# Kernel optimization log

Hardware: AMD Instinct MI355X
Metric: run time of the kernel (lower is better)

The kernel has to match this reference:

```python
import jax, jax.numpy as jnp
import numpy as np

N_T = 2_000_000      # terrain nodes
E_SEQ = 2_000_000    # sequence edges
E_AS = 2_000_000     # assignment edges
N_TOR = 1_000_000    # torus nodes
E_TR = 8_000_000     # transport edges
TD, OD, PD, N_OPS = 4, 3, 1, 4  # terrain dim, torus dim, polarity dim, num operators


def setup_inputs() -> dict:
    key = jax.random.key(0)
    ks = jax.random.split(key, 12)
    inp = {
        "x_terrain": jax.random.normal(ks[0], (N_T, TD), jnp.float32),
        "polarity": jax.random.normal(ks[1], (E_AS, PD), jnp.float32),
        "x_torus": jax.random.normal(ks[2], (N_TOR, OD), jnp.float32),
        "seq_ei": jax.random.randint(ks[3], (2, E_SEQ), 0, N_T),
        "assign_src": jax.random.randint(ks[4], (E_AS,), 0, N_T),
        "assign_dst": jax.random.randint(ks[5], (E_AS,), 0, N_OPS),
        "tr_ei": jax.random.randint(ks[6], (2, E_TR), 0, N_TOR),
        # learned params (nn.Linear convention: y = x @ W.T + b)
        "W_seq": jax.random.normal(ks[7], (TD, TD), jnp.float32) * 0.5,      # SequenceConv.lin, no bias
        "op_W": jax.random.normal(ks[8], (N_OPS, TD, TD + PD), jnp.float32) * 0.4,
        "op_b": jax.random.normal(ks[9], (N_OPS, TD), jnp.float32) * 0.1,
        "gate_W": jax.random.normal(ks[10], (2 * OD, 1), jnp.float32) * 0.4,  # TransportConv.gate
        "gate_b": jax.random.normal(ks[11], (1,), jnp.float32) * 0.1,
    }
    return inp


def _engine_fwd(x_terrain, polarity, x_torus, W_seq, op_W, op_b, gate_W, gate_b,
                seq_ei, assign_src, assign_dst, tr_ei):
    # 1) SequenceConv: add-aggregated linear message along terrain cycle, residual add
    msg = x_terrain[seq_ei[0]] @ W_seq.T                       # [E_seq, TD]
    agg = jnp.zeros_like(x_terrain).at[seq_ei[1]].add(msg)     # scatter-add to dst
    x_t = x_terrain + agg

    # 2) per-node operator transform: first assignment edge per source node
    E = assign_src.shape[0]
    pos = jnp.arange(E, dtype=jnp.int32)
    first = jax.ops.segment_min(pos, assign_src, num_segments=x_t.shape[0])  # fill = int32 max
    has = first < E                                            # nodes with >=1 assignment
    fe = jnp.clip(first, 0, E - 1)
    op_idx = jnp.clip(assign_dst[fe], 0, op_W.shape[0] - 1)    # [N_T]
    pol = polarity[fe]                                         # [N_T, 1]
    inp = jnp.concatenate([x_t, pol], axis=-1)                 # [N_T, TD+1]
    out = jnp.einsum('nij,nj->ni', op_W[op_idx], inp) + op_b[op_idx]
    x_t = jnp.where(has[:, None], out, x_t)

    # 3) TransportConv: sigmoid-gated mean aggregation over torus edges, residual add
    src, dst = tr_ei[0], tr_ei[1]
    xi, xj = x_torus[dst], x_torus[src]
    gate = jax.nn.sigmoid(jnp.concatenate([xi, xj], axis=-1) @ gate_W + gate_b)  # [E_tr,1]
    m = gate * xj
    s = jax.ops.segment_sum(m, dst, num_segments=x_torus.shape[0])
    cnt = jax.ops.segment_sum(jnp.ones((m.shape[0],), m.dtype), dst,
                              num_segments=x_torus.shape[0])
    x_tor = x_torus + s / jnp.maximum(cnt, 1.0)[:, None]
    return x_t, x_tor


def reference(x_terrain, polarity, x_torus, seq_ei, assign_src, assign_dst, tr_ei,
              W_seq, op_W, op_b, gate_W, gate_b):
    return _engine_fwd(x_terrain, polarity, x_torus, W_seq, op_W, op_b, gate_W, gate_b,
                       seq_ei, assign_src, assign_dst, tr_ei)
```

## Files before the change

kernel.cpp:

```cpp
#include <hip/hip_runtime.h>
#include <hip/hip_fp16.h>
#include <math.h>

#define N_T   2000000
#define E_SEQ 2000000
#define E_AS  2000000
#define N_TOR 1000000
#define E_TR  8000000
#define NREP  8

typedef unsigned long long u64;

__device__ __forceinline__ long long center_field(u64 t, int bits) {
    long long h = 1LL << (bits - 1);
    return (long long)((t & ((1ULL << bits) - 1)) ^ (u64)h) - h;
}

__device__ __forceinline__ unsigned xcc_id() {
    return __builtin_amdgcn_s_getreg((3 << 11) | 20) & 7u;
}

__global__ __launch_bounds__(256) void initA_kernel(ulonglong2* __restrict__ a,
                                                    ulonglong2* __restrict__ b) {
    long long i = (long long)blockIdx.x * blockDim.x + threadIdx.x;
    if (i < 2500000LL) a[i] = make_ulonglong2(0, 0);
    else if (i < 4000000LL) b[i - 2500000LL] = make_ulonglong2(0, 0);
}

__global__ __launch_bounds__(256) void prep_kernel(
        const float* __restrict__ x_torus,
        const float* __restrict__ gate_W, const float* __restrict__ gate_b,
        u64* __restrict__ src_pk, float* __restrict__ yi_arr) {
    int n = blockIdx.x * blockDim.x + threadIdx.x;
    if (n >= N_TOR) return;
    const float* x = x_torus + (size_t)n * 3;
    float x0 = x[0], x1 = x[1], x2 = x[2];
    float yi = fmaf(x0, gate_W[0], fmaf(x1, gate_W[1], x2 * gate_W[2]));
    float yj = fmaf(x0, gate_W[3], fmaf(x1, gate_W[4], fmaf(x2, gate_W[5], gate_b[0])));
    unsigned short u0, u1, u2, u3;
    __half h;
    h = __float2half(x0); __builtin_memcpy(&u0, &h, 2);
    h = __float2half(x1); __builtin_memcpy(&u1, &h, 2);
    h = __float2half(x2); __builtin_memcpy(&u2, &h, 2);
    h = __float2half(yj); __builtin_memcpy(&u3, &h, 2);
    src_pk[n] = (u64)u0 | ((u64)u1 << 16) | ((u64)u2 << 32) | ((u64)u3 << 48);
    yi_arr[n] = yi;
}

__global__ __launch_bounds__(256) void tr_kernel(
        const int* __restrict__ tr_src, const int* __restrict__ tr_dst,
        const u64* __restrict__ src_pk, const float* __restrict__ yi_arr,
        u64* rep_ws, u64* rep_out) {
    int e = blockIdx.x * blockDim.x + threadIdx.x;
    if (e >= E_TR) return;
    int si = __builtin_nontemporal_load(tr_src + e);
    int di = __builtin_nontemporal_load(tr_dst + e);
    u64 s = __builtin_nontemporal_load(src_pk + si);
    unsigned short u0 = (unsigned short)s, u1 = (unsigned short)(s >> 16),
                   u2 = (unsigned short)(s >> 32), u3 = (unsigned short)(s >> 48);
    __half h0, h1, h2, h3;
    __builtin_memcpy(&h0, &u0, 2); __builtin_memcpy(&h1, &u1, 2);
    __builtin_memcpy(&h2, &u2, 2); __builtin_memcpy(&h3, &u3, 2);
    float x0 = __half2float(h0), x1 = __half2float(h1), x2 = __half2float(h2);
    float z = yi_arr[di] + __half2float(h3);
    float g = 1.0f / (1.0f + __expf(-z));
    long long f0 = __float2int_rn(g * x0 * 128.0f);
    long long f1 = __float2int_rn(g * x1 * 128.0f);
    long long f2 = __float2int_rn(g * x2 * 128.0f);
    long long pk = f0 + (f1 << 17) + (f2 << 34) + (1LL << 51);
    unsigned r = xcc_id();
    u64* rep = (r < 5) ? rep_ws + (size_t)r * N_TOR
                       : rep_out + (size_t)(r - 5) * N_TOR;
    __hip_atomic_fetch_add(&rep[di], (u64)pk, __ATOMIC_RELAXED,
                           __HIP_MEMORY_SCOPE_WORKGROUP);
}

__global__ __launch_bounds__(256) void reduce_kernel(
        const u64* rep_ws, const u64* rep_out, u64* tor_sum) {
    int n = blockIdx.x * blockDim.x + threadIdx.x;
    if (n >= N_TOR) return;
    u64 t = 0;
    #pragma unroll
    for (int r = 0; r < 5; ++r) t += rep_ws[(size_t)r * N_TOR + n];
    #pragma unroll
    for (int r = 0; r < 3; ++r) t += rep_out[(size_t)r * N_TOR + n];
    tor_sum[n] = t;
}

__global__ __launch_bounds__(256) void initB_kernel(ulonglong2* __restrict__ ws) {
    long long i = (long long)blockIdx.x * blockDim.x + threadIdx.x;
    if (i >= 2000000LL) return;
    u64 v = (i * 2 < (long long)N_T) ? 0ULL : ~0ULL;
    ws[i] = make_ulonglong2(v, v);
}

__global__ __launch_bounds__(256) void sa_kernel(
        const float4* __restrict__ x_terrain,
        const int* __restrict__ seq_src, const int* __restrict__ seq_dst,
        const float* __restrict__ W_seq, u64* __restrict__ agg_pk,
        const int* __restrict__ assign_src, const int* __restrict__ assign_dst,
        const float* __restrict__ polarity, u64* __restrict__ first_pk) {
    int i = blockIdx.x * blockDim.x + threadIdx.x;
    if (i < E_SEQ) {
        int e = i;
        int s = __builtin_nontemporal_load(seq_src + e);
        int d = __builtin_nontemporal_load(seq_dst + e);
        float4 x = x_terrain[s];
        float m0 = fmaf(x.x, W_seq[0],  fmaf(x.y, W_seq[1],  fmaf(x.z, W_seq[2],  x.w * W_seq[3])));
        float m1 = fmaf(x.x, W_seq[4],  fmaf(x.y, W_seq[5],  fmaf(x.z, W_seq[6],  x.w * W_seq[7])));
        float m2 = fmaf(x.x, W_seq[8],  fmaf(x.y, W_seq[9],  fmaf(x.z, W_seq[10], x.w * W_seq[11])));
        float m3 = fmaf(x.x, W_seq[12], fmaf(x.y, W_seq[13], fmaf(x.z, W_seq[14], x.w * W_seq[15])));
        long long f0 = __float2int_rn(m0 * 256.0f);
        long long f1 = __float2int_rn(m1 * 256.0f);
        long long f2 = __float2int_rn(m2 * 256.0f);
        long long f3 = __float2int_rn(m3 * 256.0f);
        long long pk = f0 + (f1 << 16) + (f2 << 32) + (f3 << 48);
        atomicAdd(&agg_pk[d], (u64)pk);
    } else if (i < E_SEQ + E_AS) {
        int e = i - E_SEQ;
        int op = __builtin_nontemporal_load(assign_dst + e) & 3;
        __half h = __float2half(__builtin_nontemporal_load(polarity + e));
        unsigned short hb;
        __builtin_memcpy(&hb, &h, 2);
        u64 key = ((u64)e << 18) | ((u64)op << 16) | (u64)hb;
        atomicMin(&first_pk[__builtin_nontemporal_load(assign_src + e)], key);
    }
}

__global__ __launch_bounds__(256) void node_kernel(
        const float4* __restrict__ x_terrain,
        const u64* __restrict__ agg_pk,
        const u64* __restrict__ first_pk,
        const float* __restrict__ op_W, const float* __restrict__ op_b,
        float4* __restrict__ out_xt,
        const float* __restrict__ x_torus,
        const u64* __restrict__ tor_sum,
        float* __restrict__ out_tor) {
    int i = blockIdx.x * blockDim.x + threadIdx.x;
    if (i < N_T) {
        int n = i;
        float4 x = x_terrain[n];
        u64 t = agg_pk[n];
        long long m0 = center_field(t, 16); t = (t - (u64)m0) >> 16;
        long long m1 = center_field(t, 16); t = (t - (u64)m1) >> 16;
        long long m2 = center_field(t, 16); t = (t - (u64)m2) >> 16;
        long long m3 = center_field(t, 16);
        const float inv = 1.0f / 256.0f;
        x.x += (float)m0 * inv; x.y += (float)m1 * inv;
        x.z += (float)m2 * inv; x.w += (float)m3 * inv;
        u64 fp = first_pk[n];
        if ((fp >> 18) < (u64)E_AS) {
            int op = (int)((fp >> 16) & 3);
            unsigned short hb = (unsigned short)(fp & 0xFFFF);
            __half h;
            __builtin_memcpy(&h, &hb, 2);
            float pol = __half2float(h);
            const float* W = op_W + op * 20;
            const float* b = op_b + op * 4;
            float4 o;
            o.x = fmaf(x.x, W[0],  fmaf(x.y, W[1],  fmaf(x.z, W[2],  fmaf(x.w, W[3],  fmaf(pol, W[4],  b[0])))));
            o.y = fmaf(x.x, W[5],  fmaf(x.y, W[6],  fmaf(x.z, W[7],  fmaf(x.w, W[8],  fmaf(pol, W[9],  b[1])))));
            o.z = fmaf(x.x, W[10], fmaf(x.y, W[11], fmaf(x.z, W[12], fmaf(x.w, W[13], fmaf(pol, W[14], b[2])))));
            o.w = fmaf(x.x, W[15], fmaf(x.y, W[16], fmaf(x.z, W[17], fmaf(x.w, W[18], fmaf(pol, W[19], b[3])))));
            x = o;
        }
        out_xt[n] = x;
    } else if (i < N_T + N_TOR) {
        int n = i - N_T;
        u64 t = tor_sum[n];
        long long m0 = center_field(t, 17); t = (t - (u64)m0) >> 17;
        long long m1 = center_field(t, 17); t = (t - (u64)m1) >> 17;
        long long m2 = center_field(t, 17); t = (t - (u64)m2) >> 17;
        float cnt = (float)(t & 0x1FFF);
        float inv = (1.0f / 128.0f) / fmaxf(cnt, 1.0f);
        size_t b = (size_t)n * 3;
        out_tor[b + 0] = x_torus[b + 0] + (float)m0 * inv;
        out_tor[b + 1] = x_torus[b + 1] + (float)m1 * inv;
        out_tor[b + 2] = x_torus[b + 2] + (float)m2 * inv;
    }
}

extern "C" void kernel_launch(void* const* d_in, const int* in_sizes, int n_in,
                              void* d_out, int out_size, void* d_ws, size_t ws_size,
                              hipStream_t stream) {
    const float* x_terrain  = (const float*)d_in[0];
    const float* polarity   = (const float*)d_in[1];
    const float* x_torus    = (const float*)d_in[2];
    const int*   seq_ei     = (const int*)  d_in[3];
    const int*   assign_src = (const int*)  d_in[4];
    const int*   assign_dst = (const int*)  d_in[5];
    const int*   tr_ei      = (const int*)  d_in[6];
    const float* W_seq      = (const float*)d_in[7];
    const float* op_W       = (const float*)d_in[8];
    const float* op_b       = (const float*)d_in[9];
    const float* gate_W     = (const float*)d_in[10];
    const float* gate_b     = (const float*)d_in[11];

    float* out_xt  = (float*)d_out;
    float* out_tor = (float*)d_out + (size_t)N_T * 4;

    u64* wsu      = (u64*)d_ws;
    u64* rep_ws   = wsu;
    u64* agg_pk   = wsu;
    u64* first_pk = wsu + N_T;
    u64* tor_sum  = wsu + 2 * (size_t)N_T;
    u64* rep_out  = (u64*)d_out;
    u64* src_pk   = (u64*)d_out + 3 * (size_t)N_TOR;
    float* yi_arr = (float*)((u64*)d_out + 4 * (size_t)N_TOR);

    const int B = 256;
    initA_kernel<<<(4000000 + B - 1) / B, B, 0, stream>>>(
        (ulonglong2*)rep_ws, (ulonglong2*)rep_out);
    prep_kernel<<<(N_TOR + B - 1) / B, B, 0, stream>>>(
        x_torus, gate_W, gate_b, src_pk, yi_arr);
    tr_kernel<<<(E_TR + B - 1) / B, B, 0, stream>>>(
        tr_ei, tr_ei + E_TR, src_pk, yi_arr, rep_ws, rep_out);
    reduce_kernel<<<(N_TOR + B - 1) / B, B, 0, stream>>>(
        rep_ws, rep_out, tor_sum);
    initB_kernel<<<(2000000 + B - 1) / B, B, 0, stream>>>((ulonglong2*)wsu);
    sa_kernel<<<((E_SEQ + E_AS) + B - 1) / B, B, 0, stream>>>(
        (const float4*)x_terrain, seq_ei, seq_ei + E_SEQ, W_seq, agg_pk,
        assign_src, assign_dst, polarity, first_pk);
    const long long total_n = (long long)N_T + N_TOR;
    node_kernel<<<(int)((total_n + B - 1) / B), B, 0, stream>>>(
        (const float4*)x_terrain, agg_pk, first_pk, op_W, op_b, (float4*)out_xt,
        x_torus, tor_sum, out_tor);
}
```

Baseline: 737.6 us.

## Replace replicated global atomics for transport conv with bucketed counting-sort scatter

The transport aggregation drops per-XCC replicated global 64-bit atomics plus a reduce pass. In their place, edges are binned by destination range (histogram, scan, scatter into per-bucket record arrays). Each bucket is then reduced in LDS with shared-memory atomics and written straight to the output, so the torus finalisation leaves node_kernel. This trades random global atomics for an extra pass over the edge stream, 12-bit clamped fixed-point fields, and a single-block scan whose serial prefix sum could become a bottleneck.

Result: slower. 799.7 us (+8.4%).

```diff
diff --git a/kernel.cpp b/kernel.cpp
--- a/kernel.cpp
+++ b/kernel.cpp
@@ -7,84 +7,161 @@
 #define E_AS  2000000
 #define N_TOR 1000000
 #define E_TR  8000000
-#define NREP  8
+
+#define BKT_SHIFT 11
+#define BKT_RANGE 2048
+#define NBKT 489
+#define HIST_BLOCKS 512
+#define CHUNK 4096
+#define NCHUNK ((E_TR + CHUNK - 1) / CHUNK)
+#define NSPILL_A 4850000u
 
 typedef unsigned long long u64;
+typedef unsigned int u32;
 
 __device__ __forceinline__ long long center_field(u64 t, int bits) {
     long long h = 1LL << (bits - 1);
     return (long long)((t & ((1ULL << bits) - 1)) ^ (u64)h) - h;
 }
-
-__device__ __forceinline__ unsigned xcc_id() {
-    return __builtin_amdgcn_s_getreg((3 << 11) | 20) & 7u;
-}
-
-__global__ __launch_bounds__(256) void initA_kernel(ulonglong2* __restrict__ a,
-                                                    ulonglong2* __restrict__ b) {
-    long long i = (long long)blockIdx.x * blockDim.x + threadIdx.x;
-    if (i < 2500000LL) a[i] = make_ulonglong2(0, 0);
-    else if (i < 4000000LL) b[i - 2500000LL] = make_ulonglong2(0, 0);
-}
-
-__global__ __launch_bounds__(256) void prep_kernel(
+__device__ __forceinline__ int sext12(int v) { return ((v & 0xFFF) ^ 0x800) - 0x800; }
+
+__global__ __launch_bounds__(256) void hist_prep_kernel(
+        const int* __restrict__ tr_dst, u32* __restrict__ bhist,
         const float* __restrict__ x_torus,
         const float* __restrict__ gate_W, const float* __restrict__ gate_b,
         u64* __restrict__ src_pk, float* __restrict__ yi_arr) {
-    int n = blockIdx.x * blockDim.x + threadIdx.x;
-    if (n >= N_TOR) return;
-    const float* x = x_torus + (size_t)n * 3;
-    float x0 = x[0], x1 = x[1], x2 = x[2];
-    float yi = fmaf(x0, gate_W[0], fmaf(x1, gate_W[1], x2 * gate_W[2]));
-    float yj = fmaf(x0, gate_W[3], fmaf(x1, gate_W[4], fmaf(x2, gate_W[5], gate_b[0])));
-    unsigned short u0, u1, u2, u3;
-    __half h;
-    h = __float2half(x0); __builtin_memcpy(&u0, &h, 2);
-    h = __float2half(x1); __builtin_memcpy(&u1, &h, 2);
-    h = __float2half(x2); __builtin_memcpy(&u2, &h, 2);
-    h = __float2half(yj); __builtin_memcpy(&u3, &h, 2);
-    src_pk[n] = (u64)u0 | ((u64)u1 << 16) | ((u64)u2 << 32) | ((u64)u3 << 48);
-    yi_arr[n] = yi;
-}
-
-__global__ __launch_bounds__(256) void tr_kernel(
+    if (blockIdx.x < HIST_BLOCKS) {
+        __shared__ u32 h[NBKT];
+        for (int i = threadIdx.x; i < NBKT; i += 256) h[i] = 0;
+        __syncthreads();
+        for (long long e = (long long)blockIdx.x * 256 + threadIdx.x;
+             e < E_TR; e += (long long)HIST_BLOCKS * 256) {
+            int di = __builtin_nontemporal_load(tr_dst + e);
+            atomicAdd(&h[di >> BKT_SHIFT], 1u);
+        }
+        __syncthreads();
+        for (int i = threadIdx.x; i < NBKT; i += 256)
+            bhist[(size_t)blockIdx.x * NBKT + i] = h[i];
+    } else {
+        int n = (blockIdx.x - HIST_BLOCKS) * 256 + threadIdx.x;
+        if (n >= N_TOR) return;
+        const float* x = x_torus + (size_t)n * 3;
+        float x0 = x[0], x1 = x[1], x2 = x[2];
+        float yi = fmaf(x0, gate_W[0], fmaf(x1, gate_W[1], x2 * gate_W[2]));
+        float yj = fmaf(x0, gate_W[3], fmaf(x1, gate_W[4], fmaf(x2, gate_W[5], gate_b[0])));
+        unsigned short u0, u1, u2, u3;
+        __half h;
+        h = __float2half(x0); __builtin_memcpy(&u0, &h, 2);
+        h = __float2half(x1); __builtin_memcpy(&u1, &h, 2);
+        h = __float2half(x2); __builtin_memcpy(&u2, &h, 2);
+        h = __float2half(yj); __builtin_memcpy(&u3, &h, 2);
+        src_pk[n] = (u64)u0 | ((u64)u1 << 16) | ((u64)u2 << 32) | ((u64)u3 << 48);
+        yi_arr[n] = yi;
+    }
+}
+
+__global__ __launch_bounds__(256) void scan_kernel(
+        const u32* __restrict__ bhist, u32* __restrict__ base,
+        u32* __restrict__ cursors) {
+    __shared__ u32 tot[NBKT];
+    for (int b = threadIdx.x; b < NBKT; b += 256) {
+        u32 s = 0;
+        for (int k = 0; k < HIST_BLOCKS; ++k) s += bhist[(size_t)k * NBKT + b];
+        tot[b] = s;
+    }
+    __syncthreads();
+    if (threadIdx.x == 0) {
+        u32 acc = 0;
+        for (int b = 0; b < NBKT; ++b) { base[b] = acc; acc += tot[b]; }
+        base[NBKT] = acc;
+    }
+    __syncthreads();
+    for (int b = threadIdx.x; b < NBKT; b += 256) cursors[b * 8] = base[b];
+}
+
+__global__ __launch_bounds__(256) void scatter_kernel(
         const int* __restrict__ tr_src, const int* __restrict__ tr_dst,
         const u64* __restrict__ src_pk, const float* __restrict__ yi_arr,
-        u64* rep_ws, u64* rep_out) {
-    int e = blockIdx.x * blockDim.x + threadIdx.x;
-    if (e >= E_TR) return;
-    int si = __builtin_nontemporal_load(tr_src + e);
-    int di = __builtin_nontemporal_load(tr_dst + e);
-    u64 s = __builtin_nontemporal_load(src_pk + si);
-    unsigned short u0 = (unsigned short)s, u1 = (unsigned short)(s >> 16),
-                   u2 = (unsigned short)(s >> 32), u3 = (unsigned short)(s >> 48);
-    __half h0, h1, h2, h3;
-    __builtin_memcpy(&h0, &u0, 2); __builtin_memcpy(&h1, &u1, 2);
-    __builtin_memcpy(&h2, &u2, 2); __builtin_memcpy(&h3, &u3, 2);
-    float x0 = __half2float(h0), x1 = __half2float(h1), x2 = __half2float(h2);
-    float z = yi_arr[di] + __half2float(h3);
-    float g = 1.0f / (1.0f + __expf(-z));
-    long long f0 = __float2int_rn(g * x0 * 128.0f);
-    long long f1 = __float2int_rn(g * x1 * 128.0f);
-    long long f2 = __float2int_rn(g * x2 * 128.0f);
-    long long pk = f0 + (f1 << 17) + (f2 << 34) + (1LL << 51);
-    unsigned r = xcc_id();
-    u64* rep = (r < 5) ? rep_ws + (size_t)r * N_TOR
-                       : rep_out + (size_t)(r - 5) * N_TOR;
-    __hip_atomic_fetch_add(&rep[di], (u64)pk, __ATOMIC_RELAXED,
-                           __HIP_MEMORY_SCOPE_WORKGROUP);
-}
-
-__global__ __launch_bounds__(256) void reduce_kernel(
-        const u64* rep_ws, const u64* rep_out, u64* tor_sum) {
-    int n = blockIdx.x * blockDim.x + threadIdx.x;
-    if (n >= N_TOR) return;
-    u64 t = 0;
-    #pragma unroll
-    for (int r = 0; r < 5; ++r) t += rep_ws[(size_t)r * N_TOR + n];
-    #pragma unroll
-    for (int r = 0; r < 3; ++r) t += rep_out[(size_t)r * N_TOR + n];
-    tor_sum[n] = t;
+        u32* __restrict__ cursors,
+        u64* __restrict__ spillA, u64* __restrict__ spillB) {
+    __shared__ u32 h[NBKT];
+    __shared__ u32 sbase[NBKT];
+    long long e0 = (long long)blockIdx.x * CHUNK;
+    int nE = (int)(((long long)E_TR - e0) < CHUNK ? ((long long)E_TR - e0) : CHUNK);
+    for (int i = threadIdx.x; i < NBKT; i += 256) h[i] = 0;
+    __syncthreads();
+    for (int i = threadIdx.x; i < nE; i += 256) {
+        int di = tr_dst[e0 + i];
+        atomicAdd(&h[di >> BKT_SHIFT], 1u);
+    }
+    __syncthreads();
+    for (int b = threadIdx.x; b < NBKT; b += 256) {
+        u32 c = h[b];
+        sbase[b] = c ? atomicAdd(&cursors[b * 8], c) : 0u;
+        h[b] = 0;
+    }
+    __syncthreads();
+    for (int i = threadIdx.x; i < nE; i += 256) {
+        long long e = e0 + i;
+        int si = tr_src[e];
+        int di = tr_dst[e];
+        int bk = di >> BKT_SHIFT;
+        u64 s = src_pk[si];
+        unsigned short u0 = (unsigned short)s, u1 = (unsigned short)(s >> 16),
+                       u2 = (unsigned short)(s >> 32), u3 = (unsigned short)(s >> 48);
+        __half h0, h1, h2, h3;
+        __builtin_memcpy(&h0, &u0, 2); __builtin_memcpy(&h1, &u1, 2);
+        __builtin_memcpy(&h2, &u2, 2); __builtin_memcpy(&h3, &u3, 2);
+        float x0 = __half2float(h0), x1 = __half2float(h1), x2 = __half2float(h2);
+        float z = yi_arr[di] + __half2float(h3);
+        float g = 1.0f / (1.0f + __expf(-z));
+        int f0 = __float2int_rn(g * x0 * 128.0f);
+        int f1 = __float2int_rn(g * x1 * 128.0f);
+        int f2 = __float2int_rn(g * x2 * 128.0f);
+        f0 = f0 > 2047 ? 2047 : (f0 < -2047 ? -2047 : f0);
+        f1 = f1 > 2047 ? 2047 : (f1 < -2047 ? -2047 : f1);
+        f2 = f2 > 2047 ? 2047 : (f2 < -2047 ? -2047 : f2);
+        u32 rank = atomicAdd(&h[bk], 1u);
+        u32 slot = sbase[bk] + rank;
+        u64 rec = (u64)(f0 & 0xFFF) | ((u64)(f1 & 0xFFF) << 12)
+                | ((u64)(f2 & 0xFFF) << 24) | ((u64)(di & (BKT_RANGE - 1)) << 36);
+        if (slot < NSPILL_A) spillA[slot] = rec;
+        else                 spillB[slot - NSPILL_A] = rec;
+    }
+}
+
+__global__ __launch_bounds__(256) void bucket_kernel(
+        const u32* __restrict__ base,
+        const u64* __restrict__ spillA, const u64* __restrict__ spillB,
+        const float* __restrict__ x_torus, float* __restrict__ out_tor) {
+    __shared__ int s0[BKT_RANGE], s1[BKT_RANGE], s2[BKT_RANGE], sc[BKT_RANGE];
+    for (int i = threadIdx.x; i < BKT_RANGE; i += 256) {
+        s0[i] = 0; s1[i] = 0; s2[i] = 0; sc[i] = 0;
+    }
+    __syncthreads();
+    int b = blockIdx.x;
+    u32 lo = base[b], hi = base[b + 1];
+    for (u32 s = lo + threadIdx.x; s < hi; s += 256) {
+        u64 r = (s < NSPILL_A) ? spillA[s] : spillB[s - NSPILL_A];
+        int f0 = sext12((int)(r & 0xFFF));
+        int f1 = sext12((int)((r >> 12) & 0xFFF));
+        int f2 = sext12((int)((r >> 24) & 0xFFF));
+        int l  = (int)((r >> 36) & (BKT_RANGE - 1));
+        atomicAdd(&s0[l], f0); atomicAdd(&s1[l], f1);
+        atomicAdd(&s2[l], f2); atomicAdd(&sc[l], 1);
+    }
+    __syncthreads();
+    int n0 = b << BKT_SHIFT;
+    for (int i = threadIdx.x; i < BKT_RANGE; i += 256) {
+        int n = n0 + i;
+        if (n < N_TOR) {
+            float inv = (1.0f / 128.0f) / fmaxf((float)sc[i], 1.0f);
+            size_t p = (size_t)n * 3;
+            out_tor[p + 0] = x_torus[p + 0] + (float)s0[i] * inv;
+            out_tor[p + 1] = x_torus[p + 1] + (float)s1[i] * inv;
+            out_tor[p + 2] = x_torus[p + 2] + (float)s2[i] * inv;
+        }
+    }
 }
 
 __global__ __launch_bounds__(256) void initB_kernel(ulonglong2* __restrict__ ws) {
@@ -132,52 +209,35 @@
         const u64* __restrict__ agg_pk,
         const u64* __restrict__ first_pk,
         const float* __restrict__ op_W, const float* __restrict__ op_b,
-        float4* __restrict__ out_xt,
-        const float* __restrict__ x_torus,
-        const u64* __restrict__ tor_sum,
-        float* __restrict__ out_tor) {
-    int i = blockIdx.x * blockDim.x + threadIdx.x;
-    if (i < N_T) {
-        int n = i;
-        float4 x = x_terrain[n];
-        u64 t = agg_pk[n];
-        long long m0 = center_field(t, 16); t = (t - (u64)m0) >> 16;
-        long long m1 = center_field(t, 16); t = (t - (u64)m1) >> 16;
-        long long m2 = center_field(t, 16); t = (t - (u64)m2) >> 16;
-        long long m3 = center_field(t, 16);
-        const float inv = 1.0f / 256.0f;
-        x.x += (float)m0 * inv; x.y += (float)m1 * inv;
-        x.z += (float)m2 * inv; x.w += (float)m3 * inv;
-        u64 fp = first_pk[n];
-        if ((fp >> 18) < (u64)E_AS) {
-            int op = (int)((fp >> 16) & 3);
-            unsigned short hb = (unsigned short)(fp & 0xFFFF);
-            __half h;
-            __builtin_memcpy(&h, &hb, 2);
-            float pol = __half2float(h);
-            const float* W = op_W + op * 20;
-            const float* b = op_b + op * 4;
-            float4 o;
-            o.x = fmaf(x.x, W[0],  fmaf(x.y, W[1],  fmaf(x.z, W[2],  fmaf(x.w, W[3],  fmaf(pol, W[4],  b[0])))));
-            o.y = fmaf(x.x, W[5],  fmaf(x.y, W[6],  fmaf(x.z, W[7],  fmaf(x.w, W[8],  fmaf(pol, W[9],  b[1])))));
-            o.z = fmaf(x.x, W[10], fmaf(x.y, W[11], fmaf(x.z, W[12], fmaf(x.w, W[13], fmaf(pol, W[14], b[2])))));
-            o.w = fmaf(x.x, W[15], fmaf(x.y, W[16], fmaf(x.z, W[17], fmaf(x.w, W[18], fmaf(pol, W[19], b[3])))));
-            x = o;
-        }
-        out_xt[n] = x;
-    } else if (i < N_T + N_TOR) {
-        int n = i - N_T;
-        u64 t = tor_sum[n];
-        long long m0 = center_field(t, 17); t = (t - (u64)m0) >> 17;
-        long long m1 = center_field(t, 17); t = (t - (u64)m1) >> 17;
-        long long m2 = center_field(t, 17); t = (t - (u64)m2) >> 17;
-        float cnt = (float)(t & 0x1FFF);
-        float inv = (1.0f / 128.0f) / fmaxf(cnt, 1.0f);
-        size_t b = (size_t)n * 3;
-        out_tor[b + 0] = x_torus[b + 0] + (float)m0 * inv;
-        out_tor[b + 1] = x_torus[b + 1] + (float)m1 * inv;
-        out_tor[b + 2] = x_torus[b + 2] + (float)m2 * inv;
-    }
+        float4* __restrict__ out_xt) {
+    int n = blockIdx.x * blockDim.x + threadIdx.x;
+    if (n >= N_T) return;
+    float4 x = x_terrain[n];
+    u64 t = agg_pk[n];
+    long long m0 = center_field(t, 16); t = (t - (u64)m0) >> 16;
+    long long m1 = center_field(t, 16); t = (t - (u64)m1) >> 16;
+    long long m2 = center_field(t, 16); t = (t - (u64)m2) >> 16;
+    long long m3 = center_field(t, 16);
+    const float inv = 1.0f / 256.0f;
+    x.x += (float)m0 * inv; x.y += (float)m1 * inv;
+    x.z += (float)m2 * inv; x.w += (float)m3 * inv;
+    u64 fp = first_pk[n];
+    if ((fp >> 18) < (u64)E_AS) {
+        int op = (int)((fp >> 16) & 3);
+        unsigned short hb = (unsigned short)(fp & 0xFFFF);
+        __half h;
+        __builtin_memcpy(&h, &hb, 2);
+        float pol = __half2float(h);
+        const float* W = op_W + op * 20;
+        const float* b = op_b + op * 4;
+        float4 o;
+        o.x = fmaf(x.x, W[0],  fmaf(x.y, W[1],  fmaf(x.z, W[2],  fmaf(x.w, W[3],  fmaf(pol, W[4],  b[0])))));
+        o.y = fmaf(x.x, W[5],  fmaf(x.y, W[6],  fmaf(x.z, W[7],  fmaf(x.w, W[8],  fmaf(pol, W[9],  b[1])))));
+        o.z = fmaf(x.x, W[10], fmaf(x.y, W[11], fmaf(x.z, W[12], fmaf(x.w, W[13], fmaf(pol, W[14], b[2])))));
+        o.w = fmaf(x.x, W[15], fmaf(x.y, W[16], fmaf(x.z, W[17], fmaf(x.w, W[18], fmaf(pol, W[19], b[3])))));
+        x = o;
+    }
+    out_xt[n] = x;
 }
 
 extern "C" void kernel_launch(void* const* d_in, const int* in_sizes, int n_in,
@@ -199,30 +259,29 @@
     float* out_xt  = (float*)d_out;
     float* out_tor = (float*)d_out + (size_t)N_T * 4;
 
-    u64* wsu      = (u64*)d_ws;
-    u64* rep_ws   = wsu;
-    u64* agg_pk   = wsu;
-    u64* first_pk = wsu + N_T;
-    u64* tor_sum  = wsu + 2 * (size_t)N_T;
-    u64* rep_out  = (u64*)d_out;
-    u64* src_pk   = (u64*)d_out + 3 * (size_t)N_TOR;
-    float* yi_arr = (float*)((u64*)d_out + 4 * (size_t)N_TOR);
+    u64* spillA   = (u64*)d_ws;
+    char* tail    = (char*)d_ws + (size_t)NSPILL_A * 8;
+    u32* bhist    = (u32*)tail;
+    u32* base     = (u32*)(tail + (size_t)HIST_BLOCKS * NBKT * 4);
+    u32* cursors  = (u32*)(tail + (size_t)HIST_BLOCKS * NBKT * 4 + 2048);
+    u64* spillB   = (u64*)d_out;
+    u64* src_pk   = (u64*)((char*)d_out + 32000000);
+    float* yi_arr = (float*)((char*)d_out + 40000000);
+    u64* agg_pk   = (u64*)d_ws;
+    u64* first_pk = agg_pk + N_T;
 
     const int B = 256;
-    initA_kernel<<<(4000000 + B - 1) / B, B, 0, stream>>>(
-        (ulonglong2*)rep_ws, (ulonglong2*)rep_out);
-    prep_kernel<<<(N_TOR + B - 1) / B, B, 0, stream>>>(
-        x_torus, gate_W, gate_b, src_pk, yi_arr);
-    tr_kernel<<<(E_TR + B - 1) / B, B, 0, stream>>>(
-        tr_ei, tr_ei + E_TR, src_pk, yi_arr, rep_ws, rep_out);
-    reduce_kernel<<<(N_TOR + B - 1) / B, B, 0, stream>>>(
-        rep_ws, rep_out, tor_sum);
-    initB_kernel<<<(2000000 + B - 1) / B, B, 0, stream>>>((ulonglong2*)wsu);
+    const int prep_blocks = (N_TOR + B - 1) / B;
+    hist_prep_kernel<<<HIST_BLOCKS + prep_blocks, B, 0, stream>>>(
+        tr_ei + E_TR, bhist, x_torus, gate_W, gate_b, src_pk, yi_arr);
+    scan_kernel<<<1, B, 0, stream>>>(bhist, base, cursors);
+    scatter_kernel<<<NCHUNK, B, 0, stream>>>(
+        tr_ei, tr_ei + E_TR, src_pk, yi_arr, cursors, spillA, spillB);
+    bucket_kernel<<<NBKT, B, 0, stream>>>(base, spillA, spillB, x_torus, out_tor);
+    initB_kernel<<<(2000000 + B - 1) / B, B, 0, stream>>>((ulonglong2*)d_ws);
     sa_kernel<<<((E_SEQ + E_AS) + B - 1) / B, B, 0, stream>>>(
         (const float4*)x_terrain, seq_ei, seq_ei + E_SEQ, W_seq, agg_pk,
         assign_src, assign_dst, polarity, first_pk);
-    const long long total_n = (long long)N_T + N_TOR;
-    node_kernel<<<(int)((total_n + B - 1) / B), B, 0, stream>>>(
-        (const float4*)x_terrain, agg_pk, first_pk, op_W, op_b, (float4*)out_xt,
-        x_torus, tor_sum, out_tor);
-}
+    node_kernel<<<(N_T + B - 1) / B, B, 0, stream>>>(
+        (const float4*)x_terrain, agg_pk, first_pk, op_W, op_b, (float4*)out_xt);
+}
```

## Bucket transport edges by destination range and consume per-XCC partitions

Applied to the files above, without the earlier changes.

Replaces the per-XCC replicated atomic accumulators for the torus transport scatter with a two-phase scheme. A build kernel computes gated messages, packs them into 12-bit fixed-point records tagged with the destination, and bins them into eight destination buckets via block-local staging. A consume kernel then has each XCC atomically accumulate only the bucket for its node range, so atomics stay local to one XCC's cache. The change also drops the replica reduce and init kernels and moves the torus finalization into the sa kernel. In exchange it writes and rereads an extra 64 MB record stream, reduces message precision through 12-bit clamping, and depends on xcc_id being 0-7 and on an overflow buffer.

Result: slower. 1.173 ms (+59.0%).

```diff
diff --git a/kernel.cpp b/kernel.cpp
--- a/kernel.cpp
+++ b/kernel.cpp
@@ -7,32 +7,42 @@
 #define E_AS  2000000
 #define N_TOR 1000000
 #define E_TR  8000000
-#define NREP  8
+
+#define NB 8
+#define BKT_NODES 125000
+#define C_BKT 983040u
+#define OVF_CAP 262144u
+#define CHUNK 2048
+#define NCHUNK ((E_TR + CHUNK - 1) / CHUNK)
+
+#define C_CUR    0
+#define C_OVF    8
+#define C_RCLAIM 16
+#define C_OCLAIM 24
 
 typedef unsigned long long u64;
+typedef unsigned int u32;
 
 __device__ __forceinline__ long long center_field(u64 t, int bits) {
     long long h = 1LL << (bits - 1);
     return (long long)((t & ((1ULL << bits) - 1)) ^ (u64)h) - h;
 }
-
+__device__ __forceinline__ long long sext12(int v) {
+    return (long long)(((v & 0xFFF) ^ 0x800) - 0x800);
+}
 __device__ __forceinline__ unsigned xcc_id() {
     return __builtin_amdgcn_s_getreg((3 << 11) | 20) & 7u;
-}
-
-__global__ __launch_bounds__(256) void initA_kernel(ulonglong2* __restrict__ a,
-                                                    ulonglong2* __restrict__ b) {
-    long long i = (long long)blockIdx.x * blockDim.x + threadIdx.x;
-    if (i < 2500000LL) a[i] = make_ulonglong2(0, 0);
-    else if (i < 4000000LL) b[i - 2500000LL] = make_ulonglong2(0, 0);
 }
 
 __global__ __launch_bounds__(256) void prep_kernel(
         const float* __restrict__ x_torus,
         const float* __restrict__ gate_W, const float* __restrict__ gate_b,
-        u64* __restrict__ src_pk, float* __restrict__ yi_arr) {
+        u64* __restrict__ src_pk, __half* __restrict__ yi_h,
+        u64* __restrict__ tor_acc, u32* __restrict__ ctrl) {
     int n = blockIdx.x * blockDim.x + threadIdx.x;
+    if (n < 64) ctrl[n] = 0;
     if (n >= N_TOR) return;
+    tor_acc[n] = 0ULL;
     const float* x = x_torus + (size_t)n * 3;
     float x0 = x[0], x1 = x[1], x2 = x[2];
     float yi = fmaf(x0, gate_W[0], fmaf(x1, gate_W[1], x2 * gate_W[2]));
@@ -44,47 +54,141 @@
     h = __float2half(x2); __builtin_memcpy(&u2, &h, 2);
     h = __float2half(yj); __builtin_memcpy(&u3, &h, 2);
     src_pk[n] = (u64)u0 | ((u64)u1 << 16) | ((u64)u2 << 32) | ((u64)u3 << 48);
-    yi_arr[n] = yi;
-}
-
-__global__ __launch_bounds__(256) void tr_kernel(
+    yi_h[n] = __float2half(yi);
+}
+
+__global__ __launch_bounds__(256) void build_kernel(
         const int* __restrict__ tr_src, const int* __restrict__ tr_dst,
-        const u64* __restrict__ src_pk, const float* __restrict__ yi_arr,
-        u64* rep_ws, u64* rep_out) {
-    int e = blockIdx.x * blockDim.x + threadIdx.x;
-    if (e >= E_TR) return;
-    int si = __builtin_nontemporal_load(tr_src + e);
-    int di = __builtin_nontemporal_load(tr_dst + e);
-    u64 s = __builtin_nontemporal_load(src_pk + si);
-    unsigned short u0 = (unsigned short)s, u1 = (unsigned short)(s >> 16),
-                   u2 = (unsigned short)(s >> 32), u3 = (unsigned short)(s >> 48);
-    __half h0, h1, h2, h3;
-    __builtin_memcpy(&h0, &u0, 2); __builtin_memcpy(&h1, &u1, 2);
-    __builtin_memcpy(&h2, &u2, 2); __builtin_memcpy(&h3, &u3, 2);
-    float x0 = __half2float(h0), x1 = __half2float(h1), x2 = __half2float(h2);
-    float z = yi_arr[di] + __half2float(h3);
-    float g = 1.0f / (1.0f + __expf(-z));
-    long long f0 = __float2int_rn(g * x0 * 128.0f);
-    long long f1 = __float2int_rn(g * x1 * 128.0f);
-    long long f2 = __float2int_rn(g * x2 * 128.0f);
-    long long pk = f0 + (f1 << 17) + (f2 << 34) + (1LL << 51);
-    unsigned r = xcc_id();
-    u64* rep = (r < 5) ? rep_ws + (size_t)r * N_TOR
-                       : rep_out + (size_t)(r - 5) * N_TOR;
-    __hip_atomic_fetch_add(&rep[di], (u64)pk, __ATOMIC_RELAXED,
-                           __HIP_MEMORY_SCOPE_WORKGROUP);
-}
-
-__global__ __launch_bounds__(256) void reduce_kernel(
-        const u64* rep_ws, const u64* rep_out, u64* tor_sum) {
-    int n = blockIdx.x * blockDim.x + threadIdx.x;
-    if (n >= N_TOR) return;
-    u64 t = 0;
+        const u64* __restrict__ src_pk, const __half* __restrict__ yi_h,
+        u32* __restrict__ ctrl, u64* __restrict__ recA, u64* __restrict__ recB,
+        u64* __restrict__ ovf) {
+    __shared__ u32 cnt[NB];
+    __shared__ u32 lbase[NB + 1];
+    __shared__ u32 gbase[NB];
+    __shared__ u64 stage[CHUNK];
+    const long long e0 = (long long)blockIdx.x * CHUNK;
+    const int nE = (int)((((long long)E_TR - e0) < CHUNK) ? ((long long)E_TR - e0) : CHUNK);
+    if (threadIdx.x < NB) cnt[threadIdx.x] = 0;
+    __syncthreads();
+    u64 rec[8]; int bk[8];
     #pragma unroll
-    for (int r = 0; r < 5; ++r) t += rep_ws[(size_t)r * N_TOR + n];
+    for (int j = 0; j < 8; ++j) {
+        int i = threadIdx.x + j * 256;
+        bk[j] = -1;
+        if (i < nE) {
+            long long e = e0 + i;
+            int si = __builtin_nontemporal_load(tr_src + e);
+            int di = __builtin_nontemporal_load(tr_dst + e);
+            u64 s = src_pk[si];
+            unsigned short u0 = (unsigned short)s, u1 = (unsigned short)(s >> 16),
+                           u2 = (unsigned short)(s >> 32), u3 = (unsigned short)(s >> 48);
+            __half h0, h1, h2, h3;
+            __builtin_memcpy(&h0, &u0, 2); __builtin_memcpy(&h1, &u1, 2);
+            __builtin_memcpy(&h2, &u2, 2); __builtin_memcpy(&h3, &u3, 2);
+            float x0 = __half2float(h0), x1 = __half2float(h1), x2 = __half2float(h2);
+            float z = __half2float(yi_h[di]) + __half2float(h3);
+            float g = 1.0f / (1.0f + __expf(-z));
+            int f0 = __float2int_rn(g * x0 * 128.0f);
+            int f1 = __float2int_rn(g * x1 * 128.0f);
+            int f2 = __float2int_rn(g * x2 * 128.0f);
+            f0 = f0 > 2047 ? 2047 : (f0 < -2047 ? -2047 : f0);
+            f1 = f1 > 2047 ? 2047 : (f1 < -2047 ? -2047 : f1);
+            f2 = f2 > 2047 ? 2047 : (f2 < -2047 ? -2047 : f2);
+            rec[j] = (u64)(f0 & 0xFFF) | ((u64)(f1 & 0xFFF) << 12)
+                   | ((u64)(f2 & 0xFFF) << 24) | ((u64)di << 36);
+            int b = di / BKT_NODES;
+            bk[j] = b;
+            atomicAdd(&cnt[b], 1u);
+        }
+    }
+    __syncthreads();
+    if (threadIdx.x == 0) {
+        u32 a = 0;
+        for (int b = 0; b < NB; ++b) { lbase[b] = a; a += cnt[b]; }
+        lbase[NB] = a;
+    }
+    __syncthreads();
+    if (threadIdx.x < NB) {
+        u32 c = cnt[threadIdx.x];
+        gbase[threadIdx.x] = c ? atomicAdd(&ctrl[C_CUR + threadIdx.x], c) : 0u;
+        cnt[threadIdx.x] = 0;
+    }
+    __syncthreads();
     #pragma unroll
-    for (int r = 0; r < 3; ++r) t += rep_out[(size_t)r * N_TOR + n];
-    tor_sum[n] = t;
+    for (int j = 0; j < 8; ++j) if (bk[j] >= 0) {
+        u32 p = lbase[bk[j]] + atomicAdd(&cnt[bk[j]], 1u);
+        stage[p] = rec[j];
+    }
+    __syncthreads();
+    int total = (int)lbase[NB];
+    for (int s = threadIdx.x; s < total; s += 256) {
+        int b = 0;
+        while (s >= (int)lbase[b + 1]) ++b;
+        u32 g = gbase[b] + (u32)(s - (int)lbase[b]);
+        u64 r = stage[s];
+        if (g < C_BKT) {
+            u64* dst = (b < 5) ? recA + (size_t)b * C_BKT + g
+                               : recB + (size_t)(b - 5) * C_BKT + g;
+            __builtin_nontemporal_store(r, dst);
+        } else {
+            u32 o = atomicAdd(&ctrl[C_OVF], 1u);
+            if (o < OVF_CAP) __builtin_nontemporal_store(r, ovf + o);
+        }
+    }
+}
+
+__global__ __launch_bounds__(256) void consume_kernel(
+        u32* __restrict__ ctrl, const u64* __restrict__ recA,
+        const u64* __restrict__ recB, const u64* __restrict__ ovf,
+        u64* tor_acc) {
+    const int b = (int)xcc_id();
+    const int tid = threadIdx.x;
+    __shared__ u32 sh;
+    const int wlo = b * BKT_NODES, whi = wlo + BKT_NODES;
+    u32 size = ctrl[C_CUR + b];
+    if (size > C_BKT) size = C_BKT;
+    const u64* rp = (b < 5) ? recA + (size_t)b * C_BKT
+                            : recB + (size_t)(b - 5) * C_BKT;
+    for (;;) {
+        __syncthreads();
+        if (tid == 0) sh = atomicAdd(&ctrl[C_RCLAIM + b], 1u);
+        __syncthreads();
+        u32 st = sh * (u32)CHUNK;
+        if (st >= size) break;
+        u32 en = st + CHUNK; if (en > size) en = size;
+        for (u32 s = st + tid; s < en; s += 256) {
+            u64 r = __builtin_nontemporal_load(rp + s);
+            int d = (int)(r >> 36);
+            if (d < wlo || d >= whi) continue;
+            long long f0 = sext12((int)(r & 0xFFF));
+            long long f1 = sext12((int)((r >> 12) & 0xFFF));
+            long long f2 = sext12((int)((r >> 24) & 0xFFF));
+            u64 pk = (u64)(f0 + (f1 << 17) + (f2 << 34) + (1LL << 51));
+            __hip_atomic_fetch_add(&tor_acc[d], pk, __ATOMIC_RELAXED,
+                                   __HIP_MEMORY_SCOPE_WORKGROUP);
+        }
+    }
+    u32 ovf_n = ctrl[C_OVF];
+    if (ovf_n > OVF_CAP) ovf_n = OVF_CAP;
+    for (;;) {
+        __syncthreads();
+        if (tid == 0) sh = atomicAdd(&ctrl[C_OCLAIM + b], 1u);
+        __syncthreads();
+        u32 st = sh * (u32)CHUNK;
+        if (st >= ovf_n) break;
+        u32 en = st + CHUNK; if (en > ovf_n) en = ovf_n;
+        for (u32 s = st + tid; s < en; s += 256) {
+            u64 r = __builtin_nontemporal_load(ovf + s);
+            int d = (int)(r >> 36);
+            if (d < wlo || d >= whi) continue;
+            long long f0 = sext12((int)(r & 0xFFF));
+            long long f1 = sext12((int)((r >> 12) & 0xFFF));
+            long long f2 = sext12((int)((r >> 24) & 0xFFF));
+            u64 pk = (u64)(f0 + (f1 << 17) + (f2 << 34) + (1LL << 51));
+            __hip_atomic_fetch_add(&tor_acc[d], pk, __ATOMIC_RELAXED,
+                                   __HIP_MEMORY_SCOPE_WORKGROUP);
+        }
+    }
 }
 
 __global__ __launch_bounds__(256) void initB_kernel(ulonglong2* __restrict__ ws) {
@@ -99,7 +203,9 @@
         const int* __restrict__ seq_src, const int* __restrict__ seq_dst,
         const float* __restrict__ W_seq, u64* __restrict__ agg_pk,
         const int* __restrict__ assign_src, const int* __restrict__ assign_dst,
-        const float* __restrict__ polarity, u64* __restrict__ first_pk) {
+        const float* __restrict__ polarity, u64* __restrict__ first_pk,
+        const u64* __restrict__ tor_acc, const float* __restrict__ x_torus,
+        float* __restrict__ out_tor) {
     int i = blockIdx.x * blockDim.x + threadIdx.x;
     if (i < E_SEQ) {
         int e = i;
@@ -124,6 +230,18 @@
         __builtin_memcpy(&hb, &h, 2);
         u64 key = ((u64)e << 18) | ((u64)op << 16) | (u64)hb;
         atomicMin(&first_pk[__builtin_nontemporal_load(assign_src + e)], key);
+    } else if (i < E_SEQ + E_AS + N_TOR) {
+        int n = i - (E_SEQ + E_AS);
+        u64 t = tor_acc[n];
+        long long m0 = center_field(t, 17); t = (t - (u64)m0) >> 17;
+        long long m1 = center_field(t, 17); t = (t - (u64)m1) >> 17;
+        long long m2 = center_field(t, 17); t = (t - (u64)m2) >> 17;
+        float cnt = (float)(t & 0x1FFF);
+        float inv = (1.0f / 128.0f) / fmaxf(cnt, 1.0f);
+        size_t p = (size_t)n * 3;
+        out_tor[p + 0] = x_torus[p + 0] + (float)m0 * inv;
+        out_tor[p + 1] = x_torus[p + 1] + (float)m1 * inv;
+        out_tor[p + 2] = x_torus[p + 2] + (float)m2 * inv;
     }
 }
 
@@ -132,52 +250,35 @@
         const u64* __restrict__ agg_pk,
         const u64* __restrict__ first_pk,
         const float* __restrict__ op_W, const float* __restrict__ op_b,
-        float4* __restrict__ out_xt,
-        const float* __restrict__ x_torus,
-        const u64* __restrict__ tor_sum,
-        float* __restrict__ out_tor) {
-    int i = blockIdx.x * blockDim.x + threadIdx.x;
-    if (i < N_T) {
-        int n = i;
-        float4 x = x_terrain[n];
-        u64 t = agg_pk[n];
-        long long m0 = center_field(t, 16); t = (t - (u64)m0) >> 16;
-        long long m1 = center_field(t, 16); t = (t - (u64)m1) >> 16;
-        long long m2 = center_field(t, 16); t = (t - (u64)m2) >> 16;
-        long long m3 = center_field(t, 16);
-        const float inv = 1.0f / 256.0f;
-        x.x += (float)m0 * inv; x.y += (float)m1 * inv;
-        x.z += (float)m2 * inv; x.w += (float)m3 * inv;
-        u64 fp = first_pk[n];
-        if ((fp >> 18) < (u64)E_AS) {
-            int op = (int)((fp >> 16) & 3);
-            unsigned short hb = (unsigned short)(fp & 0xFFFF);
-            __half h;
-            __builtin_memcpy(&h, &hb, 2);
-            float pol = __half2float(h);
-            const float* W = op_W + op * 20;
-            const float* b = op_b + op * 4;
-            float4 o;
-            o.x = fmaf(x.x, W[0],  fmaf(x.y, W[1],  fmaf(x.z, W[2],  fmaf(x.w, W[3],  fmaf(pol, W[4],  b[0])))));
-            o.y = fmaf(x.x, W[5],  fmaf(x.y, W[6],  fmaf(x.z, W[7],  fmaf(x.w, W[8],  fmaf(pol, W[9],  b[1])))));
-            o.z = fmaf(x.x, W[10], fmaf(x.y, W[11], fmaf(x.z, W[12], fmaf(x.w, W[13], fmaf(pol, W[14], b[2])))));
-            o.w = fmaf(x.x, W[15], fmaf(x.y, W[16], fmaf(x.z, W[17], fmaf(x.w, W[18], fmaf(pol, W[19], b[3])))));
-            x = o;
-        }
-        out_xt[n] = x;
-    } else if (i < N_T + N_TOR) {
-        int n = i - N_T;
-        u64 t = tor_sum[n];
-        long long m0 = center_field(t, 17); t = (t - (u64)m0) >> 17;
-        long long m1 = center_field(t, 17); t = (t - (u64)m1) >> 17;
-        long long m2 = center_field(t, 17); t = (t - (u64)m2) >> 17;
-        float cnt = (float)(t & 0x1FFF);
-        float inv = (1.0f / 128.0f) / fmaxf(cnt, 1.0f);
-        size_t b = (size_t)n * 3;
-        out_tor[b + 0] = x_torus[b + 0] + (float)m0 * inv;
-        out_tor[b + 1] = x_torus[b + 1] + (float)m1 * inv;
-        out_tor[b + 2] = x_torus[b + 2] + (float)m2 * inv;
-    }
+        float4* __restrict__ out_xt) {
+    int n = blockIdx.x * blockDim.x + threadIdx.x;
+    if (n >= N_T) return;
+    float4 x = x_terrain[n];
+    u64 t = agg_pk[n];
+    long long m0 = center_field(t, 16); t = (t - (u64)m0) >> 16;
+    long long m1 = center_field(t, 16); t = (t - (u64)m1) >> 16;
+    long long m2 = center_field(t, 16); t = (t - (u64)m2) >> 16;
+    long long m3 = center_field(t, 16);
+    const float inv = 1.0f / 256.0f;
+    x.x += (float)m0 * inv; x.y += (float)m1 * inv;
+    x.z += (float)m2 * inv; x.w += (float)m3 * inv;
+    u64 fp = first_pk[n];
+    if ((fp >> 18) < (u64)E_AS) {
+        int op = (int)((fp >> 16) & 3);
+        unsigned short hb = (unsigned short)(fp & 0xFFFF);
+        __half h;
+        __builtin_memcpy(&h, &hb, 2);
+        float pol = __half2float(h);
+        const float* W = op_W + op * 20;
+        const float* b = op_b + op * 4;
+        float4 o;
+        o.x = fmaf(x.x, W[0],  fmaf(x.y, W[1],  fmaf(x.z, W[2],  fmaf(x.w, W[3],  fmaf(pol, W[4],  b[0])))));
+        o.y = fmaf(x.x, W[5],  fmaf(x.y, W[6],  fmaf(x.z, W[7],  fmaf(x.w, W[8],  fmaf(pol, W[9],  b[1])))));
+        o.z = fmaf(x.x, W[10], fmaf(x.y, W[11], fmaf(x.z, W[12], fmaf(x.w, W[13], fmaf(pol, W[14], b[2])))));
+        o.w = fmaf(x.x, W[15], fmaf(x.y, W[16], fmaf(x.z, W[17], fmaf(x.w, W[18], fmaf(pol, W[19], b[3])))));
+        x = o;
+    }
+    out_xt[n] = x;
 }
 
 extern "C" void kernel_launch(void* const* d_in, const int* in_sizes, int n_in,
@@ -199,30 +300,27 @@
     float* out_xt  = (float*)d_out;
     float* out_tor = (float*)d_out + (size_t)N_T * 4;
 
-    u64* wsu      = (u64*)d_ws;
-    u64* rep_ws   = wsu;
-    u64* agg_pk   = wsu;
-    u64* first_pk = wsu + N_T;
-    u64* tor_sum  = wsu + 2 * (size_t)N_T;
-    u64* rep_out  = (u64*)d_out;
-    u64* src_pk   = (u64*)d_out + 3 * (size_t)N_TOR;
-    float* yi_arr = (float*)((u64*)d_out + 4 * (size_t)N_TOR);
+    u64*    recA     = (u64*)d_ws;
+    u32*    ctrl     = (u32*)((char*)d_ws + 39321600);
+    u64*    tor_acc  = (u64*)d_out;
+    u64*    recB     = (u64*)((char*)d_out + 8000000);
+    u64*    ovf      = (u64*)((char*)d_out + 31592960);
+    u64*    src_pk   = (u64*)((char*)d_out + 33690112);
+    __half* yi_h     = (__half*)((char*)d_out + 41690112);
+    u64*    agg_pk   = (u64*)d_ws;
+    u64*    first_pk = agg_pk + N_T;
 
     const int B = 256;
-    initA_kernel<<<(4000000 + B - 1) / B, B, 0, stream>>>(
-        (ulonglong2*)rep_ws, (ulonglong2*)rep_out);
     prep_kernel<<<(N_TOR + B - 1) / B, B, 0, stream>>>(
-        x_torus, gate_W, gate_b, src_pk, yi_arr);
-    tr_kernel<<<(E_TR + B - 1) / B, B, 0, stream>>>(
-        tr_ei, tr_ei + E_TR, src_pk, yi_arr, rep_ws, rep_out);
-    reduce_kernel<<<(N_TOR + B - 1) / B, B, 0, stream>>>(
-        rep_ws, rep_out, tor_sum);
-    initB_kernel<<<(2000000 + B - 1) / B, B, 0, stream>>>((ulonglong2*)wsu);
-    sa_kernel<<<((E_SEQ + E_AS) + B - 1) / B, B, 0, stream>>>(
+        x_torus, gate_W, gate_b, src_pk, yi_h, tor_acc, ctrl);
+    build_kernel<<<NCHUNK, B, 0, stream>>>(
+        tr_ei, tr_ei + E_TR, src_pk, yi_h, ctrl, recA, recB, ovf);
+    consume_kernel<<<4096, B, 0, stream>>>(ctrl, recA, recB, ovf, tor_acc);
+    initB_kernel<<<(2000000 + B - 1) / B, B, 0, stream>>>((ulonglong2*)d_ws);
+    const long long sa_n = (long long)E_SEQ + E_AS + N_TOR;
+    sa_kernel<<<(int)((sa_n + B - 1) / B), B, 0, stream>>>(
         (const float4*)x_terrain, seq_ei, seq_ei + E_SEQ, W_seq, agg_pk,
-        assign_src, assign_dst, polarity, first_pk);
-    const long long total_n = (long long)N_T + N_TOR;
-    node_kernel<<<(int)((total_n + B - 1) / B), B, 0, stream>>>(
-        (const float4*)x_terrain, agg_pk, first_pk, op_W, op_b, (float4*)out_xt,
-        x_torus, tor_sum, out_tor);
-}
+        assign_src, assign_dst, polarity, first_pk, tor_acc, x_torus, out_tor);
+    node_kernel<<<(N_T + B - 1) / B, B, 0, stream>>>(
+        (const float4*)x_terrain, agg_pk, first_pk, op_W, op_b, (float4*)out_xt);
+}
```
